# Kernel optimization log

Measured on AMD Instinct MI355X. Metric: run time of the kernel, lower is better.

The kernel has to match this reference:

```python
import jax, jax.numpy as jnp
import numpy as np

D_MODEL = 1024
NUM_HEADS = 16
HEAD_DIM = D_MODEL // NUM_HEADS
THETA = 10000.0
BATCH, SEQ = 2, 2048


def rope(x, token_positions):
    # x: [b, h, s, d]; token_positions: [s]
    d = x.shape[-1]
    freqs = 1.0 / THETA ** (jnp.arange(0, d, 2, dtype=jnp.float32)[: d // 2] / d)
    ang = token_positions.astype(jnp.float32)[:, None] * freqs[None, :]  # [s, d/2]
    cos, sin = jnp.cos(ang), jnp.sin(ang)
    xr = x.reshape(*x.shape[:-1], d // 2, 2)
    x_even, x_odd = xr[..., 0], xr[..., 1]
    out_even = x_even * cos - x_odd * sin
    out_odd = x_even * sin + x_odd * cos
    return jnp.stack([out_even, out_odd], axis=-1).reshape(x.shape)


def setup_inputs() -> dict:
    key = jax.random.key(0)
    ks = jax.random.split(key, 5)
    std = np.sqrt(2.0 / (D_MODEL + D_MODEL))
    mk = lambda k: (jax.random.truncated_normal(k, -3.0, 3.0, (D_MODEL, D_MODEL), jnp.float32) * std)
    return {
        "x": jax.random.normal(ks[0], (BATCH, SEQ, D_MODEL), jnp.float32),
        "Wq": mk(ks[1]),
        "Wk": mk(ks[2]),
        "Wv": mk(ks[3]),
        "Wo": mk(ks[4]),
        "casual_mask": jnp.tril(jnp.ones((SEQ, SEQ), dtype=bool)),
        "token_positions": jnp.arange(SEQ, dtype=jnp.int32),
    }


def reference(x, Wq, Wk, Wv, Wo, casual_mask, token_positions):
    b, s, _ = x.shape
    split = lambda t: t.reshape(b, s, NUM_HEADS, HEAD_DIM).transpose(0, 2, 1, 3)
    q = split(x @ Wq.T)  # [b, h, s, d]
    k = split(x @ Wk.T)
    v = split(x @ Wv.T)
    q = rope(q, token_positions)
    k = rope(k, token_positions)
    scores = jnp.einsum("bhqd,bhkd->bhqk", q, k) / np.sqrt(HEAD_DIM)
    scores = jnp.where(casual_mask, scores, -jnp.inf)
    probs = jax.nn.softmax(scores, axis=-1)
    out = jnp.einsum("bhqk,bhkd->bhqd", probs, v)
    out = out.transpose(0, 2, 1, 3).reshape(b, s, D_MODEL)
    return out @ Wo.T
```

## Files before the change

### kernel.cpp

```cpp
#include <hip/hip_runtime.h>
#include <hip/hip_bf16.h>

#define SEQ_LEN 2048
#define NBATCH 2
#define DM 1024
#define NH 16
#define HD 64
#define NR (NBATCH * SEQ_LEN)
#define NQKV (3 * DM)
#define LDQK 2048

typedef __attribute__((ext_vector_type(8))) short bf16x8;
typedef __attribute__((ext_vector_type(4))) float f32x4;

__device__ __forceinline__ short f2b(float f) {
    __hip_bfloat16 h = __float2bfloat16(f);
    return *reinterpret_cast<short*>(&h);
}
__device__ __forceinline__ float b2f(short s) {
    union { unsigned u; float f; } x;
    x.u = ((unsigned)(unsigned short)s) << 16;
    return x.f;
}

__device__ __forceinline__ void gload_lds16(const void* g, void* l) {
    __builtin_amdgcn_global_load_lds(
        (const __attribute__((address_space(1))) unsigned int*)g,
        (__attribute__((address_space(3))) unsigned int*)l, 16, 0, 0);
}

__global__ __launch_bounds__(256) void cvt_all(
    const float* __restrict__ x,  const float* __restrict__ wq,
    const float* __restrict__ wk, const float* __restrict__ wv,
    const float* __restrict__ wo,
    __hip_bfloat16* __restrict__ xb, __hip_bfloat16* __restrict__ wqkvb,
    __hip_bfloat16* __restrict__ wob) {
    int id = blockIdx.x;
    const float* src; __hip_bfloat16* dst;
    if (id < 4096) { src = x + (size_t)id * 1024; dst = xb + (size_t)id * 1024; }
    else {
        int k = id - 4096, seg = k >> 10;
        size_t off = (size_t)(k & 1023) * 1024;
        if      (seg == 0) { src = wq + off; dst = wqkvb + off; }
        else if (seg == 1) { src = wk + off; dst = wqkvb + (1u << 20) + off; }
        else if (seg == 2) { src = wv + off; dst = wqkvb + (2u << 20) + off; }
        else               { src = wo + off; dst = wob + off; }
    }
    int i = threadIdx.x * 4;
    float4 v = *(const float4*)(src + i);
    dst[i + 0] = __float2bfloat16(v.x);
    dst[i + 1] = __float2bfloat16(v.y);
    dst[i + 2] = __float2bfloat16(v.z);
    dst[i + 3] = __float2bfloat16(v.w);
}

__device__ __forceinline__ void store_c(float* p, float v) { *p = v; }
__device__ __forceinline__ void store_c(__hip_bfloat16* p, float v) {
    *p = __float2bfloat16(v);
}

template <typename CT, bool FUSED>
__global__ __launch_bounds__(256) void gemm128(
    const __hip_bfloat16* __restrict__ A,
    const __hip_bfloat16* __restrict__ B,
    CT* __restrict__ C, int K, int ldc,
    __hip_bfloat16* __restrict__ Vtg) {
    __shared__ __hip_bfloat16 As[128 * 32];
    __shared__ __hip_bfloat16 Bs[128 * 32];
    const int t    = threadIdx.x;
    const int wave = t >> 6;
    const int lane = t & 63;
    const int quad = lane >> 4;
    const int l16  = lane & 15;
    const int wy = wave >> 1, wx = wave & 1;
    const int m0 = blockIdx.x * 128, n0 = blockIdx.y * 128;

    const int r0 = wave * 32 + (lane >> 2);
    const int c0 = (lane & 3) * 8;
    const __hip_bfloat16* Ag0 = A + (size_t)(m0 + r0) * K + c0;
    const __hip_bfloat16* Ag1 = Ag0 + (size_t)16 * K;
    const __hip_bfloat16* Bg0 = B + (size_t)(n0 + r0) * K + c0;
    const __hip_bfloat16* Bg1 = Bg0 + (size_t)16 * K;
    __hip_bfloat16* lA0 = &As[r0 * 32 + c0];
    __hip_bfloat16* lA1 = &As[(r0 + 16) * 32 + c0];
    __hip_bfloat16* lB0 = &Bs[r0 * 32 + c0];
    __hip_bfloat16* lB1 = &Bs[(r0 + 16) * 32 + c0];

    f32x4 acc[4][4];
#pragma unroll
    for (int i = 0; i < 4; i++)
#pragma unroll
        for (int j = 0; j < 4; j++) acc[i][j] = (f32x4){0.f, 0.f, 0.f, 0.f};

    for (int k0 = 0; k0 < K; k0 += 32) {
        __syncthreads();
        gload_lds16(Ag0 + k0, lA0);
        gload_lds16(Ag1 + k0, lA1);
        gload_lds16(Bg0 + k0, lB0);
        gload_lds16(Bg1 + k0, lB1);
        __syncthreads();

        bf16x8 af[4], bfr[4];
#pragma unroll
        for (int rb = 0; rb < 4; rb++)
            af[rb] = *(const bf16x8*)&As[(wy * 64 + rb * 16 + l16) * 32 + quad * 8];
#pragma unroll
        for (int cb = 0; cb < 4; cb++)
            bfr[cb] = *(const bf16x8*)&Bs[(wx * 64 + cb * 16 + l16) * 32 + quad * 8];
#pragma unroll
        for (int rb = 0; rb < 4; rb++)
#pragma unroll
            for (int cb = 0; cb < 4; cb++)
                acc[rb][cb] = __builtin_amdgcn_mfma_f32_16x16x32_bf16(
                    af[rb], bfr[cb], acc[rb][cb], 0, 0, 0);
    }

    if (!FUSED || blockIdx.y < 16) {
#pragma unroll
        for (int rb = 0; rb < 4; rb++)
#pragma unroll
            for (int r = 0; r < 4; r++) {
                size_t ro = (size_t)(m0 + wy * 64 + rb * 16 + quad * 4 + r) * ldc;
#pragma unroll
                for (int cb = 0; cb < 4; cb++)
                    store_c(&C[ro + n0 + wx * 64 + cb * 16 + l16], acc[rb][cb][r]);
            }
    } else {
#pragma unroll
        for (int rb = 0; rb < 4; rb++) {
            int row0 = m0 + wy * 64 + rb * 16 + quad * 4;
            int bb = row0 >> 11, ss = row0 & (SEQ_LEN - 1);
#pragma unroll
            for (int cb = 0; cb < 4; cb++) {
                int vcol = n0 + wx * 64 + cb * 16 + l16 - 2048;
                int hh = vcol >> 6, dd = vcol & 63;
                ushort4 u;
                u.x = (unsigned short)f2b(acc[rb][cb][0]);
                u.y = (unsigned short)f2b(acc[rb][cb][1]);
                u.z = (unsigned short)f2b(acc[rb][cb][2]);
                u.w = (unsigned short)f2b(acc[rb][cb][3]);
                *(ushort4*)(Vtg + ((size_t)(bb * NH + hh) * HD + dd) * SEQ_LEN + ss) = u;
            }
        }
    }
}

__global__ __launch_bounds__(256) void rope_kernel(
    __hip_bfloat16* __restrict__ QK, const int* __restrict__ pos) {
    int idx = blockIdx.x * 256 + threadIdx.x;
    int row  = idx >> 8;
    int tcol = idx & 255;
    int col0 = tcol * 8;
    int head = col0 >> 6;
    int i0   = (col0 & 63) >> 1;
    float p  = (float)pos[row & (SEQ_LEN - 1)];
    float scale = (head < NH) ? 0.125f : 1.0f;
    __hip_bfloat16* ptr = QK + (size_t)row * LDQK + col0;
    bf16x8 v = *(const bf16x8*)ptr;
    bf16x8 o;
#pragma unroll
    for (int k = 0; k < 4; k++) {
        float fr = __expf(-(float)(2 * (i0 + k)) * (9.210340371976184f / 64.0f));
        float ang = p * fr;
        float sn = sinf(ang), cs = cosf(ang);
        float e  = b2f(v[2 * k]);
        float od = b2f(v[2 * k + 1]);
        o[2 * k]     = f2b((e * cs - od * sn) * scale);
        o[2 * k + 1] = f2b((e * sn + od * cs) * scale);
    }
    *(bf16x8*)ptr = o;
}

__global__ __launch_bounds__(512) void attn_kernel(
    const __hip_bfloat16* __restrict__ QK,
    const __hip_bfloat16* __restrict__ Vtg,
    __hip_bfloat16* __restrict__ O) {
    __shared__ short Ps[256][72];

    const int t    = threadIdx.x;
    const int wave = t >> 6;
    const int team = wave >> 2;
    const int w4   = wave & 3;
    const int lane = t & 63;
    const int quad = lane >> 4;
    const int l16  = lane & 15;
    const int pairIdx = blockIdx.x;
    const int h    = blockIdx.y;
    const int b    = blockIdx.z;

    const int qt   = team == 0 ? pairIdx : 15 - pairIdx;
    const int row0 = qt * 128 + w4 * 32;

    bf16x8 qf[2][2];
#pragma unroll
    for (int g = 0; g < 2; g++) {
        const __hip_bfloat16* qp =
            QK + (size_t)(b * SEQ_LEN + row0 + g * 16 + l16) * LDQK + h * HD + quad * 8;
        qf[g][0] = *(const bf16x8*)qp;
        qf[g][1] = *(const bf16x8*)(qp + 32);
    }

    f32x4 o[2][4];
    float l_p[2][4];
#pragma unroll
    for (int g = 0; g < 2; g++)
#pragma unroll
        for (int r = 0; r < 4; r++) {
            o[g][r] = (f32x4){0.f, 0.f, 0.f, 0.f};
            l_p[g][r] = 0.f;
        }

    const __hip_bfloat16* kbase = QK + (size_t)(b * SEQ_LEN) * LDQK + DM + h * HD;
    const __hip_bfloat16* vbase = Vtg + (size_t)((b * NH + h) * HD) * SEQ_LEN;

    const int ktmax = (row0 + 31) >> 6;
    for (int kt = 0; kt <= ktmax; kt++) {
        bf16x8 kf[4][2], vf[4][2];
#pragma unroll
        for (int kb = 0; kb < 4; kb++) {
            const __hip_bfloat16* kp =
                kbase + (size_t)(kt * 64 + kb * 16 + l16) * LDQK + quad * 8;
            kf[kb][0] = *(const bf16x8*)kp;
            kf[kb][1] = *(const bf16x8*)(kp + 32);
        }
#pragma unroll
        for (int db = 0; db < 4; db++) {
            const __hip_bfloat16* vp =
                vbase + (size_t)(db * 16 + l16) * SEQ_LEN + kt * 64 + quad * 8;
            vf[db][0] = *(const bf16x8*)vp;
            vf[db][1] = *(const bf16x8*)(vp + 32);
        }

        f32x4 s[2][4];
#pragma unroll
        for (int g = 0; g < 2; g++)
#pragma unroll
            for (int kb = 0; kb < 4; kb++) {
                f32x4 z = {0.f, 0.f, 0.f, 0.f};
                z = __builtin_amdgcn_mfma_f32_16x16x32_bf16(qf[g][0], kf[kb][0], z, 0, 0, 0);
                z = __builtin_amdgcn_mfma_f32_16x16x32_bf16(qf[g][1], kf[kb][1], z, 0, 0, 0);
                s[g][kb] = z;
            }

        if (kt == ktmax) {
#pragma unroll
            for (int g = 0; g < 2; g++)
#pragma unroll
                for (int kb = 0; kb < 4; kb++) {
                    int key = kt * 64 + kb * 16 + l16;
#pragma unroll
                    for (int r = 0; r < 4; r++) {
                        int rowg = row0 + g * 16 + quad * 4 + r;
                        if (key > rowg) s[g][kb][r] = -1e30f;
                    }
                }
        }

#pragma unroll
        for (int g = 0; g < 2; g++)
#pragma unroll
            for (int r = 0; r < 4; r++) {
                float p0 = __expf(s[g][0][r]);
                float p1 = __expf(s[g][1][r]);
                float p2 = __expf(s[g][2][r]);
                float p3 = __expf(s[g][3][r]);
                l_p[g][r] += (p0 + p1) + (p2 + p3);
                int prow = wave * 32 + g * 16 + quad * 4 + r;
                Ps[prow][ 0 + l16] = f2b(p0);
                Ps[prow][16 + l16] = f2b(p1);
                Ps[prow][32 + l16] = f2b(p2);
                Ps[prow][48 + l16] = f2b(p3);
            }

#pragma unroll
        for (int g = 0; g < 2; g++) {
            bf16x8 pf0 = *(const bf16x8*)&Ps[wave * 32 + g * 16 + l16][quad * 8];
            bf16x8 pf1 = *(const bf16x8*)&Ps[wave * 32 + g * 16 + l16][32 + quad * 8];
#pragma unroll
            for (int db = 0; db < 4; db++) {
                o[g][db] = __builtin_amdgcn_mfma_f32_16x16x32_bf16(pf0, vf[db][0], o[g][db], 0, 0, 0);
                o[g][db] = __builtin_amdgcn_mfma_f32_16x16x32_bf16(pf1, vf[db][1], o[g][db], 0, 0, 0);
            }
        }
    }

#pragma unroll
    for (int g = 0; g < 2; g++)
#pragma unroll
        for (int r = 0; r < 4; r++) {
            float rs = l_p[g][r];
            rs += __shfl_xor(rs, 1);
            rs += __shfl_xor(rs, 2);
            rs += __shfl_xor(rs, 4);
            rs += __shfl_xor(rs, 8);
            float inv = 1.0f / rs;
            size_t ro = (size_t)(b * SEQ_LEN + row0 + g * 16 + quad * 4 + r) * DM + h * HD;
            O[ro +  0 + l16] = __float2bfloat16(o[g][0][r] * inv);
            O[ro + 16 + l16] = __float2bfloat16(o[g][1][r] * inv);
            O[ro + 32 + l16] = __float2bfloat16(o[g][2][r] * inv);
            O[ro + 48 + l16] = __float2bfloat16(o[g][3][r] * inv);
        }
}

extern "C" void kernel_launch(void* const* d_in, const int* in_sizes, int n_in,
                              void* d_out, int out_size, void* d_ws, size_t ws_size,
                              hipStream_t stream) {
    const float* x  = (const float*)d_in[0];
    const float* Wq = (const float*)d_in[1];
    const float* Wk = (const float*)d_in[2];
    const float* Wv = (const float*)d_in[3];
    const float* Wo = (const float*)d_in[4];
    const int* pos = (const int*)d_in[6];
    float* out = (float*)d_out;

    char* w = (char*)d_ws;
    const size_t MiB = 1024 * 1024;
    __hip_bfloat16* xb    = (__hip_bfloat16*)(w + 0 * MiB);
    __hip_bfloat16* Ab    = (__hip_bfloat16*)(w + 0 * MiB);
    __hip_bfloat16* Wqkvb = (__hip_bfloat16*)(w + 8 * MiB);
    __hip_bfloat16* Wob   = (__hip_bfloat16*)(w + 14 * MiB);
    __hip_bfloat16* QKb   = (__hip_bfloat16*)(w + 16 * MiB);
    __hip_bfloat16* Vtg   = (__hip_bfloat16*)(w + 32 * MiB);

    cvt_all<<<8192, 256, 0, stream>>>(x, Wq, Wk, Wv, Wo, xb, Wqkvb, Wob);

    gemm128<__hip_bfloat16, true><<<dim3(NR / 128, NQKV / 128), 256, 0, stream>>>(
        xb, Wqkvb, QKb, DM, LDQK, Vtg);

    rope_kernel<<<NR * LDQK / 8 / 256, 256, 0, stream>>>(QKb, pos);

    attn_kernel<<<dim3(8, NH, NBATCH), 512, 0, stream>>>(QKb, Vtg, Ab);

    gemm128<float, false><<<dim3(NR / 128, DM / 128), 256, 0, stream>>>(
        Ab, Wob, out, DM, DM, nullptr);
}
```

Measured before the change: 234.3 us.

## Stage K/V tiles in double-buffered LDS shared by all waves in attention

The attention kernel now copies each 64-key K and V tile into LDS once per block, using global-to-LDS loads with an XOR swizzle and double buffering. Previously every wave fetched its own K/V fragments straight from global memory, so the same data was read many times over. Each block now runs its two paired causal query tiles one after the other in a fixed 34-iteration loop, with 16 query rows per wave. This costs extra LDS space and a block-wide barrier on every iteration, and waves that have passed their causal limit sit idle during the remaining tiles.

```diff
diff --git a/kernel.cpp b/kernel.cpp
--- a/kernel.cpp
+++ b/kernel.cpp
@@ -175,131 +175,146 @@
     const __hip_bfloat16* __restrict__ QK,
     const __hip_bfloat16* __restrict__ Vtg,
     __hip_bfloat16* __restrict__ O) {
-    __shared__ short Ps[256][72];
+    __shared__ __hip_bfloat16 Ks[2][64 * 64];
+    __shared__ __hip_bfloat16 Vs[2][64 * 64];
+    __shared__ short Ps[128][72];
 
     const int t    = threadIdx.x;
     const int wave = t >> 6;
-    const int team = wave >> 2;
-    const int w4   = wave & 3;
     const int lane = t & 63;
     const int quad = lane >> 4;
     const int l16  = lane & 15;
-    const int pairIdx = blockIdx.x;
-    const int h    = blockIdx.y;
-    const int b    = blockIdx.z;
-
-    const int qt   = team == 0 ? pairIdx : 15 - pairIdx;
-    const int row0 = qt * 128 + w4 * 32;
-
-    bf16x8 qf[2][2];
-#pragma unroll
-    for (int g = 0; g < 2; g++) {
-        const __hip_bfloat16* qp =
-            QK + (size_t)(b * SEQ_LEN + row0 + g * 16 + l16) * LDQK + h * HD + quad * 8;
-        qf[g][0] = *(const bf16x8*)qp;
-        qf[g][1] = *(const bf16x8*)(qp + 32);
-    }
-
-    f32x4 o[2][4];
-    float l_p[2][4];
-#pragma unroll
-    for (int g = 0; g < 2; g++)
-#pragma unroll
-        for (int r = 0; r < 4; r++) {
-            o[g][r] = (f32x4){0.f, 0.f, 0.f, 0.f};
-            l_p[g][r] = 0.f;
-        }
+    const int pairIdx = blockIdx.x >> 5;
+    const int hb      = blockIdx.x & 31;
+    const int h       = hb & 15;
+    const int b       = hb >> 4;
+
+    const int sr  = t >> 3;
+    const int scs = (t & 7) ^ (sr & 7);
 
     const __hip_bfloat16* kbase = QK + (size_t)(b * SEQ_LEN) * LDQK + DM + h * HD;
     const __hip_bfloat16* vbase = Vtg + (size_t)((b * NH + h) * HD) * SEQ_LEN;
 
-    const int ktmax = (row0 + 31) >> 6;
-    for (int kt = 0; kt <= ktmax; kt++) {
-        bf16x8 kf[4][2], vf[4][2];
-#pragma unroll
-        for (int kb = 0; kb < 4; kb++) {
-            const __hip_bfloat16* kp =
-                kbase + (size_t)(kt * 64 + kb * 16 + l16) * LDQK + quad * 8;
-            kf[kb][0] = *(const bf16x8*)kp;
-            kf[kb][1] = *(const bf16x8*)(kp + 32);
+#define STAGE(BUF, KT)                                                          \
+    {                                                                           \
+        gload_lds16(kbase + (size_t)((KT) * 64 + sr) * LDQK + scs * 8,          \
+                    (char*)&Ks[BUF][0] + t * 16);                               \
+        gload_lds16(vbase + (size_t)sr * SEQ_LEN + (KT) * 64 + scs * 8,         \
+                    (char*)&Vs[BUF][0] + t * 16);                               \
+    }
+
+#define LDS_FRAG(BASE, RR, G)                                                   \
+    (*(const bf16x8*)((const char*)(BASE) + (RR) * 128 + ((((G) ^ ((RR) & 7))) << 4)))
+
+#define TRIP(BUF, KT)                                                           \
+    {                                                                           \
+        bf16x8 kf[4][2];                                                        \
+        _Pragma("unroll") for (int kb = 0; kb < 4; kb++) {                      \
+            int rr = kb * 16 + l16;                                             \
+            kf[kb][0] = LDS_FRAG(Ks[BUF], rr, quad);                            \
+            kf[kb][1] = LDS_FRAG(Ks[BUF], rr, quad + 4);                        \
+        }                                                                       \
+        f32x4 s[4];                                                             \
+        _Pragma("unroll") for (int kb = 0; kb < 4; kb++) {                      \
+            f32x4 z = {0.f, 0.f, 0.f, 0.f};                                     \
+            z = __builtin_amdgcn_mfma_f32_16x16x32_bf16(qf0, kf[kb][0], z, 0, 0, 0); \
+            z = __builtin_amdgcn_mfma_f32_16x16x32_bf16(qf1, kf[kb][1], z, 0, 0, 0); \
+            s[kb] = z;                                                          \
+        }                                                                       \
+        if ((KT) == ktd) {                \
+            _Pragma("unroll") for (int kb = 0; kb < 4; kb++) {                  \
+                int key = (KT) * 64 + kb * 16 + l16;                            \
+                _Pragma("unroll") for (int r = 0; r < 4; r++) {                 \
+                    int rowg = row0 + quad * 4 + r;                             \
+                    if (key > rowg) s[kb][r] = -1e30f;                          \
+                }                                                               \
+            }                                                                   \
+        }                                                                       \
+        _Pragma("unroll") for (int r = 0; r < 4; r++) {                         \
+            float p0 = __expf(s[0][r]);                                         \
+            float p1 = __expf(s[1][r]);                                         \
+            float p2 = __expf(s[2][r]);                                         \
+            float p3 = __expf(s[3][r]);                                         \
+            l_p[r] += (p0 + p1) + (p2 + p3);                                    \
+            int prow = wave * 16 + quad * 4 + r;                                \
+            Ps[prow][ 0 + l16] = f2b(p0);                                       \
+            Ps[prow][16 + l16] = f2b(p1);                                       \
+            Ps[prow][32 + l16] = f2b(p2);                                       \
+            Ps[prow][48 + l16] = f2b(p3);                                       \
+        }                                                                       \
+        bf16x8 pf0 = *(const bf16x8*)&Ps[wave * 16 + l16][quad * 8];            \
+        bf16x8 pf1 = *(const bf16x8*)&Ps[wave * 16 + l16][32 + quad * 8];       \
+        _Pragma("unroll") for (int db = 0; db < 4; db++) {                      \
+            int rr = db * 16 + l16;                                             \
+            bf16x8 vf0 = LDS_FRAG(Vs[BUF], rr, quad);                           \
+            bf16x8 vf1 = LDS_FRAG(Vs[BUF], rr, quad + 4);                       \
+            o[db] = __builtin_amdgcn_mfma_f32_16x16x32_bf16(pf0, vf0, o[db], 0, 0, 0); \
+            o[db] = __builtin_amdgcn_mfma_f32_16x16x32_bf16(pf1, vf1, o[db], 0, 0, 0); \
+        }                                                                       \
+    }
+
+#define FINALIZE()                                                              \
+    {                                                                           \
+        _Pragma("unroll") for (int r = 0; r < 4; r++) {                         \
+            float rs = l_p[r];                                                  \
+            rs += __shfl_xor(rs, 1);                                            \
+            rs += __shfl_xor(rs, 2);                                            \
+            rs += __shfl_xor(rs, 4);                                            \
+            rs += __shfl_xor(rs, 8);                                            \
+            float inv = 1.0f / rs;                                              \
+            size_t ro = (size_t)(b * SEQ_LEN + row0 + quad * 4 + r) * DM + h * HD; \
+            O[ro +  0 + l16] = __float2bfloat16(o[0][r] * inv);                 \
+            O[ro + 16 + l16] = __float2bfloat16(o[1][r] * inv);                 \
+            O[ro + 32 + l16] = __float2bfloat16(o[2][r] * inv);                 \
+            O[ro + 48 + l16] = __float2bfloat16(o[3][r] * inv);                 \
+        }                                                                       \
+    }
+
+    const int qtB = 15 - pairIdx;
+    const int n0t = 2 * qtB + 2;
+
+    int row0 = qtB * 128 + wave * 16;
+    int ktd  = row0 >> 6;
+    bf16x8 qf0, qf1;
+    {
+        const __hip_bfloat16* qp =
+            QK + (size_t)(b * SEQ_LEN + row0 + l16) * LDQK + h * HD + quad * 8;
+        qf0 = *(const bf16x8*)qp;
+        qf1 = *(const bf16x8*)(qp + 32);
+    }
+    f32x4 o[4];
+    float l_p[4];
+#pragma unroll
+    for (int r = 0; r < 4; r++) { o[r] = (f32x4){0.f, 0.f, 0.f, 0.f}; l_p[r] = 0.f; }
+
+    STAGE(0, 0);
+    for (int i = 0; i < 34; ++i) {
+        const int buf = i & 1;
+        __syncthreads();
+        if (i + 1 < 34) {
+            int inext = i + 1;
+            int ktn = (inext < n0t) ? inext : inext - n0t;
+            STAGE(buf ^ 1, ktn);
         }
-#pragma unroll
-        for (int db = 0; db < 4; db++) {
-            const __hip_bfloat16* vp =
-                vbase + (size_t)(db * 16 + l16) * SEQ_LEN + kt * 64 + quad * 8;
-            vf[db][0] = *(const bf16x8*)vp;
-            vf[db][1] = *(const bf16x8*)(vp + 32);
+        const int kt = (i < n0t) ? i : i - n0t;
+        if (kt <= ktd) TRIP(buf, kt);
+        if (i == n0t - 1) {
+            FINALIZE();
+            row0 = pairIdx * 128 + wave * 16;
+            ktd  = row0 >> 6;
+            const __hip_bfloat16* qp =
+                QK + (size_t)(b * SEQ_LEN + row0 + l16) * LDQK + h * HD + quad * 8;
+            qf0 = *(const bf16x8*)qp;
+            qf1 = *(const bf16x8*)(qp + 32);
+#pragma unroll
+            for (int r = 0; r < 4; r++) { o[r] = (f32x4){0.f, 0.f, 0.f, 0.f}; l_p[r] = 0.f; }
         }
-
-        f32x4 s[2][4];
-#pragma unroll
-        for (int g = 0; g < 2; g++)
-#pragma unroll
-            for (int kb = 0; kb < 4; kb++) {
-                f32x4 z = {0.f, 0.f, 0.f, 0.f};
-                z = __builtin_amdgcn_mfma_f32_16x16x32_bf16(qf[g][0], kf[kb][0], z, 0, 0, 0);
-                z = __builtin_amdgcn_mfma_f32_16x16x32_bf16(qf[g][1], kf[kb][1], z, 0, 0, 0);
-                s[g][kb] = z;
-            }
-
-        if (kt == ktmax) {
-#pragma unroll
-            for (int g = 0; g < 2; g++)
-#pragma unroll
-                for (int kb = 0; kb < 4; kb++) {
-                    int key = kt * 64 + kb * 16 + l16;
-#pragma unroll
-                    for (int r = 0; r < 4; r++) {
-                        int rowg = row0 + g * 16 + quad * 4 + r;
-                        if (key > rowg) s[g][kb][r] = -1e30f;
-                    }
-                }
-        }
-
-#pragma unroll
-        for (int g = 0; g < 2; g++)
-#pragma unroll
-            for (int r = 0; r < 4; r++) {
-                float p0 = __expf(s[g][0][r]);
-                float p1 = __expf(s[g][1][r]);
-                float p2 = __expf(s[g][2][r]);
-                float p3 = __expf(s[g][3][r]);
-                l_p[g][r] += (p0 + p1) + (p2 + p3);
-                int prow = wave * 32 + g * 16 + quad * 4 + r;
-                Ps[prow][ 0 + l16] = f2b(p0);
-                Ps[prow][16 + l16] = f2b(p1);
-                Ps[prow][32 + l16] = f2b(p2);
-                Ps[prow][48 + l16] = f2b(p3);
-            }
-
-#pragma unroll
-        for (int g = 0; g < 2; g++) {
-            bf16x8 pf0 = *(const bf16x8*)&Ps[wave * 32 + g * 16 + l16][quad * 8];
-            bf16x8 pf1 = *(const bf16x8*)&Ps[wave * 32 + g * 16 + l16][32 + quad * 8];
-#pragma unroll
-            for (int db = 0; db < 4; db++) {
-                o[g][db] = __builtin_amdgcn_mfma_f32_16x16x32_bf16(pf0, vf[db][0], o[g][db], 0, 0, 0);
-                o[g][db] = __builtin_amdgcn_mfma_f32_16x16x32_bf16(pf1, vf[db][1], o[g][db], 0, 0, 0);
-            }
-        }
-    }
-
-#pragma unroll
-    for (int g = 0; g < 2; g++)
-#pragma unroll
-        for (int r = 0; r < 4; r++) {
-            float rs = l_p[g][r];
-            rs += __shfl_xor(rs, 1);
-            rs += __shfl_xor(rs, 2);
-            rs += __shfl_xor(rs, 4);
-            rs += __shfl_xor(rs, 8);
-            float inv = 1.0f / rs;
-            size_t ro = (size_t)(b * SEQ_LEN + row0 + g * 16 + quad * 4 + r) * DM + h * HD;
-            O[ro +  0 + l16] = __float2bfloat16(o[g][0][r] * inv);
-            O[ro + 16 + l16] = __float2bfloat16(o[g][1][r] * inv);
-            O[ro + 32 + l16] = __float2bfloat16(o[g][2][r] * inv);
-            O[ro + 48 + l16] = __float2bfloat16(o[g][3][r] * inv);
-        }
+    }
+    FINALIZE();
+#undef STAGE
+#undef LDS_FRAG
+#undef TRIP
+#undef FINALIZE
 }
 
 extern "C" void kernel_launch(void* const* d_in, const int* in_sizes, int n_in,
@@ -329,7 +344,7 @@
 
     rope_kernel<<<NR * LDQK / 8 / 256, 256, 0, stream>>>(QKb, pos);
 
-    attn_kernel<<<dim3(8, NH, NBATCH), 512, 0, stream>>>(QKb, Vtg, Ab);
+    attn_kernel<<<256, 512, 0, stream>>>(QKb, Vtg, Ab);
 
     gemm128<float, false><<<dim3(NR / 128, DM / 128), 256, 0, stream>>>(
         Ab, Wob, out, DM, DM, nullptr);
```

Result: faster. 211.8 us (-9.6%).
